# Kernel optimization log

Measured on AMD Instinct MI355X. Metric: run time of the kernel, lower is better.

## Reference

```python
import jax, jax.numpy as jnp
import numpy as np

D = 768      # feature_dim
HD = 768     # hidden_dim
NH = 4       # num_heads
B, T1, T2 = 4, 128, 128
LN_EPS = 1e-5

def setup_inputs() -> dict:
    key = jax.random.key(0)
    ks = jax.random.split(key, 12)
    s = 0.02
    return {
        'speech_features': jax.random.normal(ks[0], (B, T1, D), jnp.float32),
        'phoneme_features': jax.random.normal(ks[1], (B, T2, D), jnp.float32),
        # per-head attention MLP: Linear(2D->HD), ReLU, Linear(HD->1); stacked over heads
        'W1': jax.random.normal(ks[2], (NH, 2 * D, HD), jnp.float32) * s,
        'b1': jnp.zeros((NH, HD), jnp.float32),
        'w2': jax.random.normal(ks[3], (NH, HD), jnp.float32) * s,
        'b2': jnp.zeros((NH,), jnp.float32),
        # fusion: Linear(2D->2HD), ReLU, Linear(2HD->D), LayerNorm(D)
        'Wf1': jax.random.normal(ks[4], (2 * D, 2 * HD), jnp.float32) * s,
        'bf1': jnp.zeros((2 * HD,), jnp.float32),
        'Wf2': jax.random.normal(ks[5], (2 * HD, D), jnp.float32) * s,
        'bf2': jnp.zeros((D,), jnp.float32),
        'ln_g': jnp.ones((D,), jnp.float32),
        'ln_b': jnp.zeros((D,), jnp.float32),
    }

def reference(speech_features, phoneme_features, W1, b1, w2, b2, Wf1, bf1, Wf2, bf2, ln_g, ln_b):
    d = speech_features.shape[-1]
    # Decompose Linear(cat([speech_t, phoneme])) = speech@W1[:d] + phoneme@W1[d:] + b1
    Wx, Wy = W1[:, :d, :], W1[:, d:, :]
    sx = jnp.einsum('btd,ndh->nbth', speech_features, Wx)   # [NH,B,T1,HD]
    py = jnp.einsum('bsd,ndh->nbsh', phoneme_features, Wy)  # [NH,B,T2,HD]
    hidden = jax.nn.relu(sx[:, :, :, None, :] + py[:, :, None, :, :]
                         + b1[:, None, None, None, :])      # [NH,B,T1,T2,HD]
    scores = jnp.einsum('nbtsh,nh->nbts', hidden, w2) + b2[:, None, None, None]
    attn = jax.nn.softmax(scores, axis=-1).mean(axis=0)     # [B,T1,T2]
    context = jnp.einsum('bts,bsd->btd', attn, phoneme_features)  # [B,T1,D]
    fused = jnp.concatenate([speech_features, context], axis=-1)  # [B,T1,2D]
    # dropout is identity in eval mode
    h = jax.nn.relu(fused @ Wf1 + bf1)
    out = h @ Wf2 + bf2
    mu = out.mean(axis=-1, keepdims=True)
    var = ((out - mu) ** 2).mean(axis=-1, keepdims=True)
    out = (out - mu) * jax.lax.rsqrt(var + LN_EPS) * ln_g + ln_b
    return out.mean(axis=1)  # [B,D]
```

## Files before the change

### kernel.cpp

```cpp
#include <hip/hip_runtime.h>
#include <cstddef>


#define D_  768
#define HD_ 768
#define NH_ 4
#define B_  4
#define T1_ 128
#define T2_ 128
#define M_  (B_*T1_)
#define LN_EPS_ 1e-5f
#define GEMM_SMEM 18944

typedef unsigned short u16;
typedef unsigned int u32;
typedef _Float16 f16;
typedef _Float16 f16x2 __attribute__((ext_vector_type(2)));
typedef __bf16 bf16x8 __attribute__((ext_vector_type(8)));
typedef float f32x4 __attribute__((ext_vector_type(4)));

__device__ __forceinline__ u16 f2bf(float f) {
    union { float f; unsigned int u; } v; v.f = f;
    unsigned int u = v.u + (0x7FFFu + ((v.u >> 16) & 1u));
    return (u16)(u >> 16);
}
__device__ __forceinline__ u32 pack_bf2(float lo, float hi) {
    return (u32)f2bf(lo) | ((u32)f2bf(hi) << 16);
}
__device__ __forceinline__ u16 f16bits(f16 h) {
    return __builtin_bit_cast(unsigned short, h);
}
__device__ __forceinline__ f16x2 bcast2(u32 u) {
    return __builtin_bit_cast(f16x2, u);
}
__device__ __forceinline__ u32 splat2(u16 h) { return (u32)h * 0x10001u; }

template<bool RELU, int MODE, bool AF32>
__device__ __forceinline__ void gemm_mfma_body(
    const void* __restrict__ Av, int lda,
    const u16* __restrict__ Bt, int ldb,
    const float* __restrict__ bias,
    void* __restrict__ C, int ldc, int K, int m0, int n0, char* smem)
{
    u16 (*As)[40] = reinterpret_cast<u16(*)[40]>(smem);
    u16 (*Bs)[40] = reinterpret_cast<u16(*)[40]>(smem + 5120);
    u16 (*Ts)[68] = reinterpret_cast<u16(*)[68]>(smem + 10240);

    const int tid = threadIdx.x;
    const int row = tid >> 2;
    const int kq  = (tid & 3) << 3;
    const int lane = tid & 63;
    const int w  = tid >> 6;
    const int wr = (w >> 1) << 5;
    const int wc = (w & 1) << 5;
    const int l16 = lane & 15;
    const int lk8 = (lane >> 4) << 3;
    const int r4  = (lane >> 4) << 2;

    const u16*   aptr16 = (const u16*)Av + (size_t)(m0 + row) * lda + kq;
    const float* aptrf  = (const float*)Av + (size_t)(m0 + row) * lda + kq;
    const u16*   bptr   = Bt + (size_t)(n0 + row) * ldb + kq;

    f32x4 acc00 = {0.f,0.f,0.f,0.f}, acc01 = {0.f,0.f,0.f,0.f};
    f32x4 acc10 = {0.f,0.f,0.f,0.f}, acc11 = {0.f,0.f,0.f,0.f};

    auto loadA = [&](int k0) -> uint4 {
        if (AF32) {
            float4 ax = *(const float4*)(aptrf + k0);
            float4 ay = *(const float4*)(aptrf + k0 + 4);
            uint4 r;
            r.x = pack_bf2(ax.x, ax.y); r.y = pack_bf2(ax.z, ax.w);
            r.z = pack_bf2(ay.x, ay.y); r.w = pack_bf2(ay.z, ay.w);
            return r;
        }
        return *(const uint4*)(aptr16 + k0);
    };

    uint4 a_nxt = loadA(0);
    uint4 b_nxt = *(const uint4*)bptr;

    for (int k0 = 0; k0 < K; k0 += 32) {
        __syncthreads();
        *(uint4*)&As[row][kq] = a_nxt;
        *(uint4*)&Bs[row][kq] = b_nxt;
        if (k0 + 32 < K) {
            a_nxt = loadA(k0 + 32);
            b_nxt = *(const uint4*)(bptr + k0 + 32);
        }
        __syncthreads();
        bf16x8 af0 = *(const bf16x8*)&As[wr + l16][lk8];
        bf16x8 af1 = *(const bf16x8*)&As[wr + 16 + l16][lk8];
        bf16x8 bf0 = *(const bf16x8*)&Bs[wc + l16][lk8];
        bf16x8 bf1 = *(const bf16x8*)&Bs[wc + 16 + l16][lk8];
        acc00 = __builtin_amdgcn_mfma_f32_16x16x32_bf16(af0, bf0, acc00, 0, 0, 0);
        acc01 = __builtin_amdgcn_mfma_f32_16x16x32_bf16(af0, bf1, acc01, 0, 0, 0);
        acc10 = __builtin_amdgcn_mfma_f32_16x16x32_bf16(af1, bf0, acc10, 0, 0, 0);
        acc11 = __builtin_amdgcn_mfma_f32_16x16x32_bf16(af1, bf1, acc11, 0, 0, 0);
    }

#define EPI_FRAG(ACC, MF, NF)                                                  \
    {                                                                          \
        const int gcol = n0 + wc + (NF)*16 + l16;                              \
        const float bv = bias ? bias[gcol] : 0.f;                              \
        float v_[4];                                                           \
        _Pragma("unroll")                                                      \
        for (int r = 0; r < 4; r++) {                                          \
            float v = ACC[r] + bv;                                             \
            if (RELU) v = fmaxf(v, 0.f);                                       \
            v_[r] = v;                                                         \
        }                                                                      \
        const int lr0 = wr + (MF)*16 + r4;                                     \
        if (MODE >= 3) {                                                       \
            const int lc = wc + (NF)*16 + l16;                                 \
            _Pragma("unroll")                                                  \
            for (int r = 0; r < 4; r++)                                        \
                Ts[lc][lr0 + r] = (MODE == 3) ? f16bits((f16)v_[r])            \
                                              : f2bf(v_[r]);                   \
        } else {                                                               \
            _Pragma("unroll")                                                  \
            for (int r = 0; r < 4; r++) {                                      \
                const size_t off = (size_t)(m0 + lr0 + r) * ldc + gcol;        \
                if (MODE == 0) ((float*)C)[off] = v_[r];                       \
                else if (MODE == 1) ((u16*)C)[off] = f2bf(v_[r]);              \
                else ((u16*)C)[off] = f16bits((f16)v_[r]);                     \
            }                                                                  \
        }                                                                      \
    }
    EPI_FRAG(acc00, 0, 0) EPI_FRAG(acc01, 0, 1)
    EPI_FRAG(acc10, 1, 0) EPI_FRAG(acc11, 1, 1)
#undef EPI_FRAG

    if (MODE >= 3) {
        __syncthreads();
        u16* cb = (u16*)C + (size_t)(m0 >> 7) * ((size_t)ldc * 128) + (m0 & 127);
#pragma unroll
        for (int u = 0; u < 4; u++) {
            const int i = tid + u * 256;
            const int hl = i >> 4;
            const int s4 = (i & 15) << 2;
            ushort4 o;
            o.x = Ts[hl][s4 + 0]; o.y = Ts[hl][s4 + 1];
            o.z = Ts[hl][s4 + 2]; o.w = Ts[hl][s4 + 3];
            *(ushort4*)(cb + (size_t)(n0 + hl) * 128 + s4) = o;
        }
    }
}

__global__ __launch_bounds__(256) void prep_kernel(
    const float* __restrict__ W1, const float* __restrict__ Wf1,
    const float* __restrict__ Wf2,
    u16* __restrict__ w1t, u16* __restrict__ wf1t, u16* __restrict__ wf2t)
{
    const int tid = threadIdx.x;
    int bid = blockIdx.x;
    const float* in; u16* outp; int tx, ty;
    if (bid < 4608) {
        const int z = bid / 1152, r = bid % 1152;
        tx = r % 24; ty = r / 24;
        in = W1 + (size_t)z * 1536 * 768; outp = w1t + (size_t)z * 768 * 1536;
    } else if (bid < 6912) {
        const int r = bid - 4608;
        tx = r % 48; ty = r / 48;
        in = Wf1; outp = wf1t;
    } else {
        const int r = bid - 6912;
        tx = r % 24; ty = r / 24;
        in = Wf2; outp = wf2t;
    }
    const int C = (bid >= 4608 && bid < 6912) ? 1536 : 768;
    const int c0 = tx * 32, r0 = ty * 32;
    __shared__ float tile[32][33];
    const int tr = tid >> 3, tc = (tid & 7) << 2;
    float4 v = *(const float4*)(in + (size_t)(r0 + tr) * C + c0 + tc);
    tile[tr][tc] = v.x; tile[tr][tc + 1] = v.y;
    tile[tr][tc + 2] = v.z; tile[tr][tc + 3] = v.w;
    __syncthreads();
    ushort4 o;
    o.x = f2bf(tile[tc + 0][tr]); o.y = f2bf(tile[tc + 1][tr]);
    o.z = f2bf(tile[tc + 2][tr]); o.w = f2bf(tile[tc + 3][tr]);
    *(ushort4*)(outp + (size_t)(c0 + tr) * 1536 + r0 + tc) = o;
}

__global__ __launch_bounds__(256) void sxpypw_kernel(
    const float* __restrict__ sp, const float* __restrict__ ph,
    const u16* __restrict__ w1t, const u16* __restrict__ wf1t,
    const float* __restrict__ b1,
    u16* __restrict__ sxf, u16* __restrict__ pyt, u16* __restrict__ pwt)
{
    __shared__ __align__(16) char smem[GEMM_SMEM];
    int job = blockIdx.x;
    if (job < 384) {
        const int n = job / 96, r = job % 96, my = r / 12, nx = r % 12;
        gemm_mfma_body<false, 2, true>(sp, 768,
            w1t + (size_t)n * 768 * 1536, 1536, b1 + n * HD_,
            sxf + (size_t)n * M_ * HD_, HD_, 768, my * 64, nx * 64, smem);
    } else if (job < 768) {
        const int j = job - 384;
        const int n = j / 96, r = j % 96, my = r / 12, nx = r % 12;
        gemm_mfma_body<false, 3, true>(ph, 768,
            w1t + (size_t)n * 768 * 1536 + 768, 1536, nullptr,
            pyt + (size_t)n * 4 * 768 * 128, 768, 768, my * 64, nx * 64, smem);
    } else {
        const int j = job - 768;
        const int b = j / 48, r = j % 48, my = r / 24, nx = r % 24;
        gemm_mfma_body<false, 4, true>(ph + (size_t)b * 128 * 768, 768,
            wf1t + 768, 1536, nullptr,
            pwt + (size_t)b * 1536 * 128, 1536, 768, my * 64, nx * 64, smem);
    }
}

__global__ __launch_bounds__(256) void scores_softmax_kernel(
    const u16* __restrict__ sxf,
    const u16* __restrict__ pyt,
    const float* __restrict__ w2,
    float* __restrict__ probs)
{
    const int bid = blockIdx.x;
    const int n = bid >> 6, b = (bid >> 4) & 3, t0 = (bid & 15) * 8;
    const int tid = threadIdx.x, lane = tid & 63, w = tid >> 6;

    __shared__ __align__(16) f16x2 sxs[8][768];
    __shared__ __align__(16) f16x2 w2s[768];

    for (int q = 0; q < 6; q++) {
        const int u = tid + q * 256;
        const int r = u / 192;
        const int h4 = (u % 192) * 4;
        ushort4 v = *(const ushort4*)(sxf + ((size_t)(n * 512 + b * 128 + t0 + r)) * 768 + h4);
        sxs[r][h4 + 0] = bcast2(splat2(v.x));
        sxs[r][h4 + 1] = bcast2(splat2(v.y));
        sxs[r][h4 + 2] = bcast2(splat2(v.z));
        sxs[r][h4 + 3] = bcast2(splat2(v.w));
    }
    for (int q = 0; q < 3; q++) {
        const int i = tid + q * 256;
        w2s[i] = bcast2(splat2(f16bits((f16)w2[n * 768 + i])));
    }
    __syncthreads();

    const f16x2* pypanel = (const f16x2*)(pyt + ((size_t)((n << 2) | b)) * 768 * 128) + lane;
    const f16x2 z2 = {(f16)0, (f16)0};

    float accA0 = 0.f, accA1 = 0.f, accB0 = 0.f, accB1 = 0.f;
    const int rA = 2 * w, rB = 2 * w + 1;

    f16x2 b0[16], b1[16];
#pragma unroll
    for (int j = 0; j < 16; j++) b0[j] = pypanel[(size_t)j * 64];
#pragma unroll
    for (int j = 0; j < 16; j++) b1[j] = pypanel[(size_t)(16 + j) * 64];

    auto compute = [&](const f16x2 (&buf)[16], int hbase) {
        f16x2 aA = z2, aB = z2;
#pragma unroll
        for (int j4 = 0; j4 < 16; j4 += 4) {
            uint4 sau = *(const uint4*)&sxs[rA][hbase + j4];
            uint4 sbu = *(const uint4*)&sxs[rB][hbase + j4];
            uint4 wvu = *(const uint4*)&w2s[hbase + j4];
            const u32 sa_[4] = {sau.x, sau.y, sau.z, sau.w};
            const u32 sb_[4] = {sbu.x, sbu.y, sbu.z, sbu.w};
            const u32 wv_[4] = {wvu.x, wvu.y, wvu.z, wvu.w};
#pragma unroll
            for (int j = 0; j < 4; j++) {
                const f16x2 pv = buf[j4 + j];
                const f16x2 wj = bcast2(wv_[j]);
                f16x2 ra = __builtin_elementwise_max(bcast2(sa_[j]) + pv, z2);
                f16x2 rb = __builtin_elementwise_max(bcast2(sb_[j]) + pv, z2);
                aA = __builtin_elementwise_fma(ra, wj, aA);
                aB = __builtin_elementwise_fma(rb, wj, aB);
            }
        }
        accA0 += (float)aA.x; accA1 += (float)aA.y;
        accB0 += (float)aB.x; accB1 += (float)aB.y;
    };

    for (int hc = 0; hc < 768; hc += 32) {
        compute(b0, hc);
        if (hc + 32 < 768) {
#pragma unroll
            for (int j = 0; j < 16; j++) b0[j] = pypanel[(size_t)(hc + 32 + j) * 64];
        }
        compute(b1, hc + 16);
        if (hc + 48 < 768) {
#pragma unroll
            for (int j = 0; j < 16; j++) b1[j] = pypanel[(size_t)(hc + 48 + j) * 64];
        }
    }

#pragma unroll
    for (int which = 0; which < 2; which++) {
        const float s0 = which ? accB0 : accA0;
        const float s1 = which ? accB1 : accA1;
        const int t = t0 + 2 * w + which;
        float mx = fmaxf(s0, s1);
#pragma unroll
        for (int off = 32; off; off >>= 1) mx = fmaxf(mx, __shfl_xor(mx, off, 64));
        const float e0 = expf(s0 - mx), e1 = expf(s1 - mx);
        float sm = e0 + e1;
#pragma unroll
        for (int off = 32; off; off >>= 1) sm += __shfl_xor(sm, off, 64);
        const float inv = 0.25f / sm;
        float2 pr; pr.x = e0 * inv; pr.y = e1 * inv;
        *(float2*)&probs[((size_t)(n * 512 + b * 128 + t)) * 128 + 2 * lane] = pr;
    }
}

__global__ __launch_bounds__(256) void gemm_ffn1_kernel(
    const float* __restrict__ speech, const float* __restrict__ probs,
    const u16* __restrict__ wf1t, const u16* __restrict__ pwt,
    const float* __restrict__ bf1, u16* __restrict__ hbuf)
{
    __shared__ __align__(16) u16 As[64][40];
    __shared__ __align__(16) u16 Bs[64][40];

    const int tid = threadIdx.x;
    const int row = tid >> 2;
    const int kq  = (tid & 3) << 3;
    const int lane = tid & 63;
    const int w  = tid >> 6;
    const int wr = (w >> 1) << 5;
    const int wc = (w & 1) << 5;
    const int l16 = lane & 15;
    const int lk8 = (lane >> 4) << 3;
    const int r4  = (lane >> 4) << 2;

    const int m0 = blockIdx.y * 64, n0 = blockIdx.x * 64;
    const int b = m0 >> 7;

    const float* arow = speech + (size_t)(m0 + row) * 768 + kq;
    const float* prow = probs + (size_t)(m0 + row) * 128 + kq;
    const u16* brow_w = wf1t + (size_t)(n0 + row) * 1536 + kq;
    const u16* brow_p = pwt + (size_t)b * 1536 * 128 + (size_t)(n0 + row) * 128 + kq;

    f32x4 acc00 = {0.f,0.f,0.f,0.f}, acc01 = {0.f,0.f,0.f,0.f};
    f32x4 acc10 = {0.f,0.f,0.f,0.f}, acc11 = {0.f,0.f,0.f,0.f};

    auto loadA = [&](int k0) -> uint4 {
        uint4 r;
        if (k0 < 768) {
            float4 ax = *(const float4*)(arow + k0);
            float4 ay = *(const float4*)(arow + k0 + 4);
            r.x = pack_bf2(ax.x, ax.y); r.y = pack_bf2(ax.z, ax.w);
            r.z = pack_bf2(ay.x, ay.y); r.w = pack_bf2(ay.z, ay.w);
        } else {
            const int ko = k0 - 768;
            float4 ax = make_float4(0.f, 0.f, 0.f, 0.f), ay = ax;
#pragma unroll
            for (int n = 0; n < 4; n++) {
                float4 u0 = *(const float4*)(prow + (size_t)n * 512 * 128 + ko);
                float4 u1 = *(const float4*)(prow + (size_t)n * 512 * 128 + ko + 4);
                ax.x += u0.x; ax.y += u0.y; ax.z += u0.z; ax.w += u0.w;
                ay.x += u1.x; ay.y += u1.y; ay.z += u1.z; ay.w += u1.w;
            }
            r.x = pack_bf2(ax.x, ax.y); r.y = pack_bf2(ax.z, ax.w);
            r.z = pack_bf2(ay.x, ay.y); r.w = pack_bf2(ay.z, ay.w);
        }
        return r;
    };
    auto loadB = [&](int k0) -> uint4 {
        if (k0 < 768) return *(const uint4*)(brow_w + k0);
        return *(const uint4*)(brow_p + (k0 - 768));
    };

    uint4 a_nxt = loadA(0);
    uint4 b_nxt = loadB(0);

    for (int k0 = 0; k0 < 896; k0 += 32) {
        __syncthreads();
        *(uint4*)&As[row][kq] = a_nxt;
        *(uint4*)&Bs[row][kq] = b_nxt;
        if (k0 + 32 < 896) {
            a_nxt = loadA(k0 + 32);
            b_nxt = loadB(k0 + 32);
        }
        __syncthreads();
        bf16x8 af0 = *(const bf16x8*)&As[wr + l16][lk8];
        bf16x8 af1 = *(const bf16x8*)&As[wr + 16 + l16][lk8];
        bf16x8 bf0 = *(const bf16x8*)&Bs[wc + l16][lk8];
        bf16x8 bf1 = *(const bf16x8*)&Bs[wc + 16 + l16][lk8];
        acc00 = __builtin_amdgcn_mfma_f32_16x16x32_bf16(af0, bf0, acc00, 0, 0, 0);
        acc01 = __builtin_amdgcn_mfma_f32_16x16x32_bf16(af0, bf1, acc01, 0, 0, 0);
        acc10 = __builtin_amdgcn_mfma_f32_16x16x32_bf16(af1, bf0, acc10, 0, 0, 0);
        acc11 = __builtin_amdgcn_mfma_f32_16x16x32_bf16(af1, bf1, acc11, 0, 0, 0);
    }

#define EPI_FFN1(ACC, MF, NF)                                                  \
    {                                                                          \
        const int gcol = n0 + wc + (NF)*16 + l16;                              \
        const float bv = bf1[gcol];                                            \
        const int lr0 = wr + (MF)*16 + r4;                                     \
        _Pragma("unroll")                                                      \
        for (int r = 0; r < 4; r++) {                                          \
            float v = fmaxf(ACC[r] + bv, 0.f);                                 \
            hbuf[(size_t)(m0 + lr0 + r) * 1536 + gcol] = f2bf(v);              \
        }                                                                      \
    }
    EPI_FFN1(acc00, 0, 0) EPI_FFN1(acc01, 0, 1)
    EPI_FFN1(acc10, 1, 0) EPI_FFN1(acc11, 1, 1)
#undef EPI_FFN1
}

__global__ __launch_bounds__(256) void gemm_ffn2_kernel(
    const u16* __restrict__ hbuf, const u16* __restrict__ wf2t,
    const float* __restrict__ bf2, float* __restrict__ outpre)
{
    __shared__ __align__(16) char smem[GEMM_SMEM];
    gemm_mfma_body<false, 0, false>(hbuf, 1536, wf2t, 1536, bf2,
                                    outpre, 768, 1536,
                                    blockIdx.y * 64, blockIdx.x * 64, smem);
}

__global__ __launch_bounds__(256) void ln_fused_kernel(
    const float* __restrict__ x, const float* __restrict__ g,
    const float* __restrict__ lb, float* __restrict__ out)
{
    const int b = blockIdx.x / 3, c = blockIdx.x % 3;
    const int tid = threadIdx.x, lane = tid & 63, w = tid >> 6;
    __shared__ float rs[T1_];
    __shared__ float Sred[4];

    float prsum = 0.f;
    for (int i = 0; i < 32; i++) {
        const int row = w * 32 + i;
        const float4* x4 = (const float4*)(x + ((size_t)(b * T1_ + row)) * D_);
        float s = 0.f, ss = 0.f;
#pragma unroll
        for (int j = 0; j < 3; j++) {
            float4 v = x4[j * 64 + lane];
            s += v.x + v.y + v.z + v.w;
            ss += v.x * v.x + v.y * v.y + v.z * v.z + v.w * v.w;
        }
#pragma unroll
        for (int off = 32; off; off >>= 1) {
            s += __shfl_xor(s, off, 64);
            ss += __shfl_xor(ss, off, 64);
        }
        if (lane == 0) {
            const float mu = s * (1.f / D_);
            const float var = ss * (1.f / D_) - mu * mu;
            const float r = rsqrtf(var + LN_EPS_);
            rs[row] = r;
            prsum += mu * r;
        }
    }
    if (lane == 0) Sred[w] = prsum;
    __syncthreads();
    const float S = Sred[0] + Sred[1] + Sred[2] + Sred[3];
    const float* xb = x + (size_t)b * T1_ * D_;
    const int d = c * 256 + tid;
    float acc = 0.f;
#pragma unroll 8
    for (int t = 0; t < T1_; t++)
        acc = fmaf(xb[(size_t)t * D_ + d], rs[t], acc);
    out[b * D_ + d] = g[d] * (acc - S) * (1.f / T1_) + lb[d];
}

extern "C" void kernel_launch(void* const* d_in, const int* in_sizes, int n_in,
                              void* d_out, int out_size, void* d_ws, size_t ws_size,
                              hipStream_t stream)
{
    const float* speech = (const float*)d_in[0];
    const float* phon   = (const float*)d_in[1];
    const float* W1     = (const float*)d_in[2];
    const float* b1     = (const float*)d_in[3];
    const float* w2     = (const float*)d_in[4];
    const float* Wf1    = (const float*)d_in[6];
    const float* bf1    = (const float*)d_in[7];
    const float* Wf2    = (const float*)d_in[8];
    const float* bf2    = (const float*)d_in[9];
    const float* ln_g   = (const float*)d_in[10];
    const float* ln_b   = (const float*)d_in[11];
    float* out = (float*)d_out;

    char* w = (char*)d_ws;
    auto alloc = [&](size_t bytes) { char* p = w; w += (bytes + 1023) & ~(size_t)1023; return p; };
    u16* w1t    = (u16*)alloc((size_t)NH_ * 768 * 1536 * 2);
    u16* wf1t   = (u16*)alloc((size_t)1536 * 1536 * 2);
    u16* wf2t   = (u16*)alloc((size_t)768 * 1536 * 2);
    u16* sxf    = (u16*)alloc((size_t)NH_ * M_ * HD_ * 2);
    u16* pyt    = (u16*)alloc((size_t)NH_ * B_ * 768 * 128 * 2);
    u16* pwt    = (u16*)alloc((size_t)B_ * 1536 * 128 * 2);
    float* probs  = (float*)alloc((size_t)NH_ * M_ * T2_ * 4);
    u16* hbuf   = (u16*)alloc((size_t)M_ * 2 * HD_ * 2);
    float* outpre = (float*)alloc((size_t)M_ * D_ * 4);

    hipLaunchKernelGGL(prep_kernel, dim3(8064), dim3(256), 0, stream,
                       W1, Wf1, Wf2, w1t, wf1t, wf2t);
    hipLaunchKernelGGL(sxpypw_kernel, dim3(960), dim3(256), 0, stream,
                       speech, phon, w1t, wf1t, b1, sxf, pyt, pwt);
    hipLaunchKernelGGL(scores_softmax_kernel, dim3(256), dim3(256), 0, stream,
                       sxf, pyt, w2, probs);
    hipLaunchKernelGGL(gemm_ffn1_kernel, dim3(24, 8), dim3(256), 0, stream,
                       speech, probs, wf1t, pwt, bf1, hbuf);
    hipLaunchKernelGGL(gemm_ffn2_kernel, dim3(12, 8), dim3(256), 0, stream,
                       hbuf, wf2t, bf2, outpre);
    hipLaunchKernelGGL(ln_fused_kernel, dim3(12), dim3(256), 0, stream,
                       outpre, ln_g, ln_b, out);
}
```

Measured before the change: 118.2 us.

## Drop weight transpose prep kernel; read fp32 weights directly and fuse FFN2 with LayerNorm

Removes the separate prep kernel that transposed and converted W1, Wf1 and Wf2 to bf16. The GEMMs now load the fp32 row-major weights directly, converting to bf16 and transposing into shared memory in the loader. The FFN2 GEMM and the LayerNorm reduction are merged into one launch, where the LN blocks spin on an atomic counter until all GEMM tiles finish. This saves one full weight-conversion pass and two launches, at the cost of uncoalesced-ish strided B loads, double fp32 weight bytes per GEMM, and a spin-wait that relies on all 108 blocks being co-resident.

```diff
diff --git a/kernel.cpp b/kernel.cpp
--- a/kernel.cpp
+++ b/kernel.cpp
@@ -3,7 +3,6 @@
 
 
 #define D_  768
-#define HD_ 768
 #define NH_ 4
 #define B_  4
 #define T1_ 128
@@ -35,10 +34,10 @@
 }
 __device__ __forceinline__ u32 splat2(u16 h) { return (u32)h * 0x10001u; }
 
-template<bool RELU, int MODE, bool AF32>
+template<bool RELU, int MODE, bool AF32, int BMODE>
 __device__ __forceinline__ void gemm_mfma_body(
     const void* __restrict__ Av, int lda,
-    const u16* __restrict__ Bt, int ldb,
+    const void* __restrict__ Bv, int ldb,
     const float* __restrict__ bias,
     void* __restrict__ C, int ldc, int K, int m0, int n0, char* smem)
 {
@@ -49,6 +48,8 @@
     const int tid = threadIdx.x;
     const int row = tid >> 2;
     const int kq  = (tid & 3) << 3;
+    const int kp  = tid >> 4;
+    const int nq  = (tid & 15) << 2;
     const int lane = tid & 63;
     const int w  = tid >> 6;
     const int wr = (w >> 1) << 5;
@@ -59,11 +60,13 @@
 
     const u16*   aptr16 = (const u16*)Av + (size_t)(m0 + row) * lda + kq;
     const float* aptrf  = (const float*)Av + (size_t)(m0 + row) * lda + kq;
-    const u16*   bptr   = Bt + (size_t)(n0 + row) * ldb + kq;
+    const u16*   bptr16 = (const u16*)Bv + (size_t)(n0 + row) * ldb + kq;
+    const float* bptrf  = (const float*)Bv + (size_t)(2 * kp) * ldb + n0 + nq;
 
     f32x4 acc00 = {0.f,0.f,0.f,0.f}, acc01 = {0.f,0.f,0.f,0.f};
     f32x4 acc10 = {0.f,0.f,0.f,0.f}, acc11 = {0.f,0.f,0.f,0.f};
 
+    uint4 a_nxt; uint4 bu; float4 bx, by;
     auto loadA = [&](int k0) -> uint4 {
         if (AF32) {
             float4 ax = *(const float4*)(aptrf + k0);
@@ -75,18 +78,29 @@
         }
         return *(const uint4*)(aptr16 + k0);
     };
-
-    uint4 a_nxt = loadA(0);
-    uint4 b_nxt = *(const uint4*)bptr;
+    auto loadB = [&](int k0) {
+        if (BMODE == 1) {
+            bx = *(const float4*)(bptrf + (size_t)k0 * ldb);
+            by = *(const float4*)(bptrf + (size_t)(k0 + 1) * ldb);
+        } else {
+            bu = *(const uint4*)(bptr16 + k0);
+        }
+    };
+
+    a_nxt = loadA(0); loadB(0);
 
     for (int k0 = 0; k0 < K; k0 += 32) {
         __syncthreads();
         *(uint4*)&As[row][kq] = a_nxt;
-        *(uint4*)&Bs[row][kq] = b_nxt;
-        if (k0 + 32 < K) {
-            a_nxt = loadA(k0 + 32);
-            b_nxt = *(const uint4*)(bptr + k0 + 32);
-        }
+        if (BMODE == 1) {
+            *(u32*)&Bs[nq + 0][2 * kp] = pack_bf2(bx.x, by.x);
+            *(u32*)&Bs[nq + 1][2 * kp] = pack_bf2(bx.y, by.y);
+            *(u32*)&Bs[nq + 2][2 * kp] = pack_bf2(bx.z, by.z);
+            *(u32*)&Bs[nq + 3][2 * kp] = pack_bf2(bx.w, by.w);
+        } else {
+            *(uint4*)&Bs[row][kq] = bu;
+        }
+        if (k0 + 32 < K) { a_nxt = loadA(k0 + 32); loadB(k0 + 32); }
         __syncthreads();
         bf16x8 af0 = *(const bf16x8*)&As[wr + l16][lk8];
         bf16x8 af1 = *(const bf16x8*)&As[wr + 16 + l16][lk8];
@@ -121,7 +135,6 @@
             for (int r = 0; r < 4; r++) {                                      \
                 const size_t off = (size_t)(m0 + lr0 + r) * ldc + gcol;        \
                 if (MODE == 0) ((float*)C)[off] = v_[r];                       \
-                else if (MODE == 1) ((u16*)C)[off] = f2bf(v_[r]);              \
                 else ((u16*)C)[off] = f16bits((f16)v_[r]);                     \
             }                                                                  \
         }                                                                      \
@@ -146,44 +159,9 @@
     }
 }
 
-__global__ __launch_bounds__(256) void prep_kernel(
-    const float* __restrict__ W1, const float* __restrict__ Wf1,
-    const float* __restrict__ Wf2,
-    u16* __restrict__ w1t, u16* __restrict__ wf1t, u16* __restrict__ wf2t)
-{
-    const int tid = threadIdx.x;
-    int bid = blockIdx.x;
-    const float* in; u16* outp; int tx, ty;
-    if (bid < 4608) {
-        const int z = bid / 1152, r = bid % 1152;
-        tx = r % 24; ty = r / 24;
-        in = W1 + (size_t)z * 1536 * 768; outp = w1t + (size_t)z * 768 * 1536;
-    } else if (bid < 6912) {
-        const int r = bid - 4608;
-        tx = r % 48; ty = r / 48;
-        in = Wf1; outp = wf1t;
-    } else {
-        const int r = bid - 6912;
-        tx = r % 24; ty = r / 24;
-        in = Wf2; outp = wf2t;
-    }
-    const int C = (bid >= 4608 && bid < 6912) ? 1536 : 768;
-    const int c0 = tx * 32, r0 = ty * 32;
-    __shared__ float tile[32][33];
-    const int tr = tid >> 3, tc = (tid & 7) << 2;
-    float4 v = *(const float4*)(in + (size_t)(r0 + tr) * C + c0 + tc);
-    tile[tr][tc] = v.x; tile[tr][tc + 1] = v.y;
-    tile[tr][tc + 2] = v.z; tile[tr][tc + 3] = v.w;
-    __syncthreads();
-    ushort4 o;
-    o.x = f2bf(tile[tc + 0][tr]); o.y = f2bf(tile[tc + 1][tr]);
-    o.z = f2bf(tile[tc + 2][tr]); o.w = f2bf(tile[tc + 3][tr]);
-    *(ushort4*)(outp + (size_t)(c0 + tr) * 1536 + r0 + tc) = o;
-}
-
 __global__ __launch_bounds__(256) void sxpypw_kernel(
     const float* __restrict__ sp, const float* __restrict__ ph,
-    const u16* __restrict__ w1t, const u16* __restrict__ wf1t,
+    const float* __restrict__ W1, const float* __restrict__ Wf1,
     const float* __restrict__ b1,
     u16* __restrict__ sxf, u16* __restrict__ pyt, u16* __restrict__ pwt)
 {
@@ -191,20 +169,20 @@
     int job = blockIdx.x;
     if (job < 384) {
         const int n = job / 96, r = job % 96, my = r / 12, nx = r % 12;
-        gemm_mfma_body<false, 2, true>(sp, 768,
-            w1t + (size_t)n * 768 * 1536, 1536, b1 + n * HD_,
-            sxf + (size_t)n * M_ * HD_, HD_, 768, my * 64, nx * 64, smem);
+        gemm_mfma_body<false, 2, true, 1>(sp, 768,
+            W1 + (size_t)n * 1536 * 768, 768, b1 + n * 768,
+            sxf + (size_t)n * M_ * 768, 768, 768, my * 64, nx * 64, smem);
     } else if (job < 768) {
         const int j = job - 384;
         const int n = j / 96, r = j % 96, my = r / 12, nx = r % 12;
-        gemm_mfma_body<false, 3, true>(ph, 768,
-            w1t + (size_t)n * 768 * 1536 + 768, 1536, nullptr,
+        gemm_mfma_body<false, 3, true, 1>(ph, 768,
+            W1 + (size_t)n * 1536 * 768 + (size_t)768 * 768, 768, nullptr,
             pyt + (size_t)n * 4 * 768 * 128, 768, 768, my * 64, nx * 64, smem);
     } else {
         const int j = job - 768;
         const int b = j / 48, r = j % 48, my = r / 24, nx = r % 24;
-        gemm_mfma_body<false, 4, true>(ph + (size_t)b * 128 * 768, 768,
-            wf1t + 768, 1536, nullptr,
+        gemm_mfma_body<false, 4, true, 1>(ph + (size_t)b * 128 * 768, 768,
+            Wf1 + (size_t)768 * 1536, 1536, nullptr,
             pwt + (size_t)b * 1536 * 128, 1536, 768, my * 64, nx * 64, smem);
     }
 }
@@ -307,7 +285,7 @@
 
 __global__ __launch_bounds__(256) void gemm_ffn1_kernel(
     const float* __restrict__ speech, const float* __restrict__ probs,
-    const u16* __restrict__ wf1t, const u16* __restrict__ pwt,
+    const float* __restrict__ Wf1, const u16* __restrict__ pwt,
     const float* __restrict__ bf1, u16* __restrict__ hbuf)
 {
     __shared__ __align__(16) u16 As[64][40];
@@ -316,6 +294,8 @@
     const int tid = threadIdx.x;
     const int row = tid >> 2;
     const int kq  = (tid & 3) << 3;
+    const int kp  = tid >> 4;
+    const int nq  = (tid & 15) << 2;
     const int lane = tid & 63;
     const int w  = tid >> 6;
     const int wr = (w >> 1) << 5;
@@ -329,12 +309,13 @@
 
     const float* arow = speech + (size_t)(m0 + row) * 768 + kq;
     const float* prow = probs + (size_t)(m0 + row) * 128 + kq;
-    const u16* brow_w = wf1t + (size_t)(n0 + row) * 1536 + kq;
+    const float* bptrf = Wf1 + (size_t)(2 * kp) * 1536 + n0 + nq;
     const u16* brow_p = pwt + (size_t)b * 1536 * 128 + (size_t)(n0 + row) * 128 + kq;
 
     f32x4 acc00 = {0.f,0.f,0.f,0.f}, acc01 = {0.f,0.f,0.f,0.f};
     f32x4 acc10 = {0.f,0.f,0.f,0.f}, acc11 = {0.f,0.f,0.f,0.f};
 
+    uint4 a_nxt; uint4 bu; float4 bx, by;
     auto loadA = [&](int k0) -> uint4 {
         uint4 r;
         if (k0 < 768) {
@@ -357,22 +338,29 @@
         }
         return r;
     };
-    auto loadB = [&](int k0) -> uint4 {
-        if (k0 < 768) return *(const uint4*)(brow_w + k0);
-        return *(const uint4*)(brow_p + (k0 - 768));
+    auto loadB = [&](int k0) {
+        if (k0 < 768) {
+            bx = *(const float4*)(bptrf + (size_t)k0 * 1536);
+            by = *(const float4*)(bptrf + (size_t)(k0 + 1) * 1536);
+        } else {
+            bu = *(const uint4*)(brow_p + (k0 - 768));
+        }
     };
 
-    uint4 a_nxt = loadA(0);
-    uint4 b_nxt = loadB(0);
+    a_nxt = loadA(0); loadB(0);
 
     for (int k0 = 0; k0 < 896; k0 += 32) {
         __syncthreads();
         *(uint4*)&As[row][kq] = a_nxt;
-        *(uint4*)&Bs[row][kq] = b_nxt;
-        if (k0 + 32 < 896) {
-            a_nxt = loadA(k0 + 32);
-            b_nxt = loadB(k0 + 32);
-        }
+        if (k0 < 768) {
+            *(u32*)&Bs[nq + 0][2 * kp] = pack_bf2(bx.x, by.x);
+            *(u32*)&Bs[nq + 1][2 * kp] = pack_bf2(bx.y, by.y);
+            *(u32*)&Bs[nq + 2][2 * kp] = pack_bf2(bx.z, by.z);
+            *(u32*)&Bs[nq + 3][2 * kp] = pack_bf2(bx.w, by.w);
+        } else {
+            *(uint4*)&Bs[row][kq] = bu;
+        }
+        if (k0 + 32 < 896) { a_nxt = loadA(k0 + 32); loadB(k0 + 32); }
         __syncthreads();
         bf16x8 af0 = *(const bf16x8*)&As[wr + l16][lk8];
         bf16x8 af1 = *(const bf16x8*)&As[wr + 16 + l16][lk8];
@@ -392,7 +380,7 @@
         _Pragma("unroll")                                                      \
         for (int r = 0; r < 4; r++) {                                          \
             float v = fmaxf(ACC[r] + bv, 0.f);                                 \
-            hbuf[(size_t)(m0 + lr0 + r) * 1536 + gcol] = f2bf(v);              \
+            hbuf[(size_t)(m0 + lr0 + r) * 1536 + gcol] = f2bf(v);   \
         }                                                                      \
     }
     EPI_FFN1(acc00, 0, 0) EPI_FFN1(acc01, 0, 1)
@@ -400,33 +388,49 @@
 #undef EPI_FFN1
 }
 
-__global__ __launch_bounds__(256) void gemm_ffn2_kernel(
-    const u16* __restrict__ hbuf, const u16* __restrict__ wf2t,
-    const float* __restrict__ bf2, float* __restrict__ outpre)
+__global__ __launch_bounds__(256) void ffn2_ln_kernel(
+    const u16* __restrict__ hbuf, const float* __restrict__ Wf2,
+    const float* __restrict__ bf2, const float* __restrict__ g,
+    const float* __restrict__ lb, float* __restrict__ outpre,
+    float* __restrict__ out, unsigned int* __restrict__ cnt)
 {
     __shared__ __align__(16) char smem[GEMM_SMEM];
-    gemm_mfma_body<false, 0, false>(hbuf, 1536, wf2t, 1536, bf2,
-                                    outpre, 768, 1536,
-                                    blockIdx.y * 64, blockIdx.x * 64, smem);
-}
-
-__global__ __launch_bounds__(256) void ln_fused_kernel(
-    const float* __restrict__ x, const float* __restrict__ g,
-    const float* __restrict__ lb, float* __restrict__ out)
-{
-    const int b = blockIdx.x / 3, c = blockIdx.x % 3;
-    const int tid = threadIdx.x, lane = tid & 63, w = tid >> 6;
-    __shared__ float rs[T1_];
-    __shared__ float Sred[4];
+    const int bid = blockIdx.x;
+    const int tid = threadIdx.x;
+
+    if (bid < 96) {
+        const int my = bid / 12, nx = bid % 12;
+        gemm_mfma_body<false, 0, false, 1>(hbuf, 1536, Wf2, 768, bf2,
+                                           outpre, 768, 1536,
+                                           my * 64, nx * 64, smem);
+        __threadfence();
+        __syncthreads();
+        if (tid == 0)
+            __hip_atomic_fetch_add(cnt, 1u, __ATOMIC_RELEASE, __HIP_MEMORY_SCOPE_AGENT);
+        return;
+    }
+
+    if (tid == 0) {
+        while (__hip_atomic_load(cnt, __ATOMIC_ACQUIRE, __HIP_MEMORY_SCOPE_AGENT) < 96u)
+            __builtin_amdgcn_s_sleep(8);
+    }
+    __syncthreads();
+    __threadfence();
+
+    const int j = bid - 96;
+    const int b = j / 3, c = j % 3;
+    const int lane = tid & 63, w = tid >> 6;
+    float* rs = reinterpret_cast<float*>(smem);
+    float* Sred = rs + 128;
 
     float prsum = 0.f;
     for (int i = 0; i < 32; i++) {
-        const int row = w * 32 + i;
-        const float4* x4 = (const float4*)(x + ((size_t)(b * T1_ + row)) * D_);
+        const int rowg = w * 32 + i;
+        const float4* x4 = (const float4*)(outpre + ((size_t)(b * T1_ + rowg)) * D_);
         float s = 0.f, ss = 0.f;
 #pragma unroll
-        for (int j = 0; j < 3; j++) {
-            float4 v = x4[j * 64 + lane];
+        for (int jj = 0; jj < 3; jj++) {
+            float4 v = x4[jj * 64 + lane];
             s += v.x + v.y + v.z + v.w;
             ss += v.x * v.x + v.y * v.y + v.z * v.z + v.w * v.w;
         }
@@ -439,14 +443,14 @@
             const float mu = s * (1.f / D_);
             const float var = ss * (1.f / D_) - mu * mu;
             const float r = rsqrtf(var + LN_EPS_);
-            rs[row] = r;
+            rs[rowg] = r;
             prsum += mu * r;
         }
     }
     if (lane == 0) Sred[w] = prsum;
     __syncthreads();
     const float S = Sred[0] + Sred[1] + Sred[2] + Sred[3];
-    const float* xb = x + (size_t)b * T1_ * D_;
+    const float* xb = outpre + (size_t)b * T1_ * D_;
     const int d = c * 256 + tid;
     float acc = 0.f;
 #pragma unroll 8
@@ -474,26 +478,21 @@
 
     char* w = (char*)d_ws;
     auto alloc = [&](size_t bytes) { char* p = w; w += (bytes + 1023) & ~(size_t)1023; return p; };
-    u16* w1t    = (u16*)alloc((size_t)NH_ * 768 * 1536 * 2);
-    u16* wf1t   = (u16*)alloc((size_t)1536 * 1536 * 2);
-    u16* wf2t   = (u16*)alloc((size_t)768 * 1536 * 2);
-    u16* sxf    = (u16*)alloc((size_t)NH_ * M_ * HD_ * 2);
+    u16* sxf    = (u16*)alloc((size_t)NH_ * M_ * 768 * 2);
     u16* pyt    = (u16*)alloc((size_t)NH_ * B_ * 768 * 128 * 2);
     u16* pwt    = (u16*)alloc((size_t)B_ * 1536 * 128 * 2);
     float* probs  = (float*)alloc((size_t)NH_ * M_ * T2_ * 4);
-    u16* hbuf   = (u16*)alloc((size_t)M_ * 2 * HD_ * 2);
+    u16* hbuf   = (u16*)alloc((size_t)M_ * 2 * 768 * 2);
     float* outpre = (float*)alloc((size_t)M_ * D_ * 4);
-
-    hipLaunchKernelGGL(prep_kernel, dim3(8064), dim3(256), 0, stream,
-                       W1, Wf1, Wf2, w1t, wf1t, wf2t);
+    unsigned int* cnt = (unsigned int*)alloc(64);
+
+    hipMemsetAsync(cnt, 0, 4, stream);
     hipLaunchKernelGGL(sxpypw_kernel, dim3(960), dim3(256), 0, stream,
-                       speech, phon, w1t, wf1t, b1, sxf, pyt, pwt);
+                       speech, phon, W1, Wf1, b1, sxf, pyt, pwt);
     hipLaunchKernelGGL(scores_softmax_kernel, dim3(256), dim3(256), 0, stream,
                        sxf, pyt, w2, probs);
     hipLaunchKernelGGL(gemm_ffn1_kernel, dim3(24, 8), dim3(256), 0, stream,
-                       speech, probs, wf1t, pwt, bf1, hbuf);
-    hipLaunchKernelGGL(gemm_ffn2_kernel, dim3(12, 8), dim3(256), 0, stream,
-                       hbuf, wf2t, bf2, outpre);
-    hipLaunchKernelGGL(ln_fused_kernel, dim3(12), dim3(256), 0, stream,
-                       outpre, ln_g, ln_b, out);
-}
+                       speech, probs, Wf1, pwt, bf1, hbuf);
+    hipLaunchKernelGGL(ffn2_ln_kernel, dim3(108), dim3(256), 0, stream,
+                       hbuf, Wf2, bf2, ln_g, ln_b, outpre, out, cnt);
+}
```

Result: slower. 151.0 us (+27.8%).
